# Performance work log

Measured on AMD Instinct MI355X. Metric: run time of the kernel, lower is better.

The kernel has to match this reference:

```python
import jax, jax.numpy as jnp
import numpy as np

B, S, D = 16, 1024, 1024   # batch, seq_len, dim_oculta
R, E = 512, 768            # n_riesgo lexicon entries, embedding dim
LN_EPS = 1e-5


def setup_inputs() -> dict:
    key = jax.random.key(0)
    ks = jax.random.split(key, 12)
    sd = 1.0 / np.sqrt(D)
    se = 1.0 / np.sqrt(E)
    return {
        "lstm_output": jax.random.normal(ks[0], (B, S, D), dtype=jnp.float32),
        "emb_riesgo": jax.random.normal(ks[1], (R, E), dtype=jnp.float32),
        "Wq": jax.random.normal(ks[2], (D, D), dtype=jnp.float32) * sd,
        "bq": jnp.zeros((D,), dtype=jnp.float32),
        "Wk": jax.random.normal(ks[3], (D, D), dtype=jnp.float32) * sd,
        "bk": jnp.zeros((D,), dtype=jnp.float32),
        "Wv": jax.random.normal(ks[4], (D, D), dtype=jnp.float32) * sd,
        "bv": jnp.zeros((D,), dtype=jnp.float32),
        "Wpr": jax.random.normal(ks[5], (E, D), dtype=jnp.float32) * se,
        "bpr": jnp.zeros((D,), dtype=jnp.float32),
        "escala": jnp.float32(1.0 / np.sqrt(D)),
        "gamma": jnp.ones((D,), dtype=jnp.float32),
        "beta": jnp.zeros((D,), dtype=jnp.float32),
    }


def reference(lstm_output, emb_riesgo, Wq, bq, Wk, bk, Wv, bv, Wpr, bpr,
              escala, gamma, beta):
    # Projections: [B,S,D]
    q = lstm_output @ Wq + bq
    k = lstm_output @ Wk + bk
    v = lstm_output @ Wv + bv

    # Risk lexicon projection: [R,D]
    riesgo_proy = emb_riesgo @ Wpr + bpr
    # Lexicon scores [B,S,R] -> max over lexicon -> sigmoid relevance [B,S,1]
    punt_lex = jnp.einsum('bsd,rd->bsr', q, riesgo_proy)
    relevancia = jax.nn.sigmoid(jnp.max(punt_lex, axis=-1, keepdims=True))

    # Hand-rolled self-attention
    scores = jnp.einsum('bsd,btd->bst', q, k) * escala   # [B,S,S]
    pesos = jax.nn.softmax(scores, axis=-1)
    contexto = jnp.einsum('bst,btd->bsd', pesos, v)      # [B,S,D]

    # Lexicon boost + LayerNorm over last dim
    x = contexto * (1.0 + relevancia)
    mu = jnp.mean(x, axis=-1, keepdims=True)
    var = jnp.mean(jnp.square(x - mu), axis=-1, keepdims=True)
    x = (x - mu) * jax.lax.rsqrt(var + LN_EPS) * gamma + beta

    # Mean pool over sequence -> [B,D]
    return jnp.mean(x, axis=1)
```

## Files before the change

### kernel.cpp

```cpp
#include <hip/hip_runtime.h>


#define BB 16
#define SS 1024
#define DD 1024
#define RR 512
#define EE 768

typedef __attribute__((ext_vector_type(4))) float f32x4;
typedef __attribute__((ext_vector_type(8))) __bf16 bf16x8;
typedef __attribute__((ext_vector_type(4))) unsigned int u32x4;

typedef __attribute__((address_space(1))) const void g_void;
typedef __attribute__((address_space(3))) void l_void;

__device__ __forceinline__ ushort f2b(float x) {
    unsigned u = __float_as_uint(x);
    u += 0x7fffu + ((u >> 16) & 1u);
    return (ushort)(u >> 16);
}

__global__ void cast_f32_bf16(const float* __restrict__ in, ushort* __restrict__ out, long n4) {
    long i = (long)blockIdx.x * blockDim.x + threadIdx.x;
    if (i >= n4) return;
    float4 v = *(const float4*)(in + i * 4);
    ushort4 o;
    o.x = f2b(v.x); o.y = f2b(v.y); o.z = f2b(v.z); o.w = f2b(v.w);
    *(ushort4*)(out + i * 4) = o;
}

__global__ void transpose_cast(const float* __restrict__ in, ushort* __restrict__ out,
                               int rows, int cols) {
    __shared__ float tile[32][33];
    const int bx = blockIdx.x * 32;
    const int by = blockIdx.y * 32;
    const int tx = threadIdx.x;
    const int ty = threadIdx.y;
#pragma unroll
    for (int i = 0; i < 32; i += 8)
        tile[ty + i][tx] = in[(long)(by + ty + i) * cols + bx + tx];
    __syncthreads();
#pragma unroll
    for (int i = 0; i < 32; i += 8)
        out[(long)(bx + ty + i) * rows + by + tx] = f2b(tile[tx][ty + i]);
}


#define VMWAIT(N) asm volatile("s_waitcnt vmcnt(" #N ")" ::: "memory")
#define BARRIER() asm volatile("s_barrier" ::: "memory")
#define LGKM0()   asm volatile("s_waitcnt lgkmcnt(0)" ::: "memory")
#define DSR(dst, addr, imm) \
    asm volatile("ds_read_b128 %0, %1 offset:" #imm : "=v"(dst) : "v"(addr))

#define STAGE(buf, mat, h, ti_) do {                                               \
    const int ti__ = (ti_) < (T - 1) ? (ti_) : (T - 1);                            \
    const ushort* sp__ = (mat) ? Bb : Ab;                                          \
    const long kb__ = (long)ti__ * 64 + scol;                                      \
    _Pragma("unroll")                                                              \
    for (int i__ = 0; i__ < 2; ++i__) {                                            \
        const int row0__ = (mat)                                                   \
            ? ((i__ * 2 + (wave >> 2)) * 64 + (h) * 32 + (wave & 3) * 8)           \
            : (i__ * 128 + (h) * 64 + wave * 8);                                   \
        __builtin_amdgcn_global_load_lds(                                          \
            (g_void*)(sp__ + (long)(row0__ + srow) * K + kb__),                    \
            (l_void*)(&lds[(buf) * 2 + (mat)][row0__ * 64]), 16, 0, 0);            \
    }                                                                              \
} while (0)

#define PHASE(curoff_, mh, nh, STAGE_STMT, WAIT_STMT) do {                         \
    if ((nh) == 0) {                                                               \
        const unsigned a0__ = abase0 + (curoff_) + (mh) * 8192;                    \
        const unsigned a1__ = abase1 + (curoff_) + (mh) * 8192;                    \
        DSR(af[0][0], a0__, 0);    DSR(af[0][1], a1__, 0);                         \
        DSR(af[1][0], a0__, 2048); DSR(af[1][1], a1__, 2048);                      \
        DSR(af[2][0], a0__, 4096); DSR(af[2][1], a1__, 4096);                      \
        DSR(af[3][0], a0__, 6144); DSR(af[3][1], a1__, 6144);                      \
    }                                                                              \
    {                                                                              \
        const unsigned b0__ = bbase0 + (curoff_) + (nh) * 4096;                    \
        const unsigned b1__ = bbase1 + (curoff_) + (nh) * 4096;                    \
        DSR(bfr[0][0], b0__, 0);    DSR(bfr[0][1], b1__, 0);                       \
        DSR(bfr[1][0], b0__, 2048); DSR(bfr[1][1], b1__, 2048);                    \
    }                                                                              \
    STAGE_STMT;                                                                    \
    BARRIER();                                                                     \
    LGKM0();                                                                       \
    __builtin_amdgcn_sched_barrier(0);                                             \
    __builtin_amdgcn_s_setprio(1);                                                 \
    _Pragma("unroll")                                                              \
    for (int mi = 0; mi < 4; ++mi)                                                 \
        _Pragma("unroll")                                                          \
        for (int ni = 0; ni < 2; ++ni) {                                           \
            acc[(mh) * 4 + mi][(nh) * 2 + ni] = __builtin_amdgcn_mfma_f32_16x16x32_bf16( \
                __builtin_bit_cast(bf16x8, af[mi][0]),                             \
                __builtin_bit_cast(bf16x8, bfr[ni][0]),                            \
                acc[(mh) * 4 + mi][(nh) * 2 + ni], 0, 0, 0);                       \
            acc[(mh) * 4 + mi][(nh) * 2 + ni] = __builtin_amdgcn_mfma_f32_16x16x32_bf16( \
                __builtin_bit_cast(bf16x8, af[mi][1]),                             \
                __builtin_bit_cast(bf16x8, bfr[ni][1]),                            \
                acc[(mh) * 4 + mi][(nh) * 2 + ni], 0, 0, 0);                       \
        }                                                                          \
    __builtin_amdgcn_s_setprio(0);                                                 \
    WAIT_STMT;                                                                     \
    BARRIER();                                                                     \
} while (0)

template <int BIAS_MODE, bool OUT_BF16, bool ROWSCALE>
__global__ __launch_bounds__(512, 2) void gemm8(
    const ushort* __restrict__ A, const ushort* __restrict__ B, void* __restrict__ C,
    const float* __restrict__ bias, const float* __restrict__ rowscale,
    const float* __restrict__ scale_ptr,
    int N, int K, int M, long sA, long sB, long sC)
{
    __shared__ ushort lds[4][16384];
    const int tid  = threadIdx.x;
    const int wave = tid >> 6;
    const int lane = tid & 63;
    const int wm = wave >> 2, wn = wave & 3;

    const int nx = gridDim.x, ny = gridDim.y;
    long flat = blockIdx.x + (long)nx * (blockIdx.y + (long)ny * blockIdx.z);
    const long nwg = (long)nx * ny * gridDim.z;
    const long cpx = nwg >> 3;
    flat = (flat & 7) * cpx + (flat >> 3);
    const int bn = (int)(flat % nx);
    const long r1 = flat / nx;
    const int bm = (int)(r1 % ny);
    const int bz = (int)(r1 / ny);

    const ushort* Ab = A + (long)bz * sA + (long)bm * 256 * K;
    const ushort* Bb = B + (long)bz * sB + (long)bn * 256 * K;
    const int T = K >> 6;

    const int srow = lane >> 3;
    const int scol = ((lane & 7) ^ srow) * 8;

    const unsigned lb = (unsigned)(unsigned long long)(void*)&lds[0][0];
    const int r15 = lane & 15;
    const int k0  = (lane >> 4) * 8;
    const int xo  = (lane & 7) * 8;
    const unsigned colA = (unsigned)((k0 ^ xo) * 2);
    const unsigned arow = (unsigned)((wm * 128 + r15) * 128);
    const unsigned brow = (unsigned)((wn * 64 + r15) * 128);
    const unsigned abase0 = lb + arow + colA;
    const unsigned abase1 = lb + arow + (colA ^ 64u);
    const unsigned bbase0 = lb + 32768u + brow + colA;
    const unsigned bbase1 = lb + 32768u + brow + (colA ^ 64u);

    f32x4 acc[8][4];
#pragma unroll
    for (int i = 0; i < 8; ++i)
#pragma unroll
        for (int j = 0; j < 4; ++j) acc[i][j] = (f32x4){0.f, 0.f, 0.f, 0.f};

    u32x4 af[4][2], bfr[2][2];

    STAGE(0, 0, 0, 0); STAGE(0, 1, 0, 0); STAGE(0, 0, 1, 0); STAGE(0, 1, 1, 0);
    STAGE(1, 0, 0, 1); STAGE(1, 1, 0, 1);
    VMWAIT(8);
    BARRIER();

    for (int t = 0; t < T; ++t) {
        const int cur = t & 1, nxt = cur ^ 1;
        const unsigned curoff = cur ? 65536u : 0u;
        PHASE(curoff, 0, 0, STAGE(nxt, 0, 1, t + 1), VMWAIT(6));
        PHASE(curoff, 0, 1, STAGE(nxt, 1, 1, t + 1), (void)0);
        PHASE(curoff, 1, 0, STAGE(cur, 0, 0, t + 2), (void)0);
        PHASE(curoff, 1, 1, STAGE(cur, 1, 0, t + 2), VMWAIT(8));
    }
    VMWAIT(0);

    const float scale = scale_ptr ? *scale_ptr : 1.0f;
    const int g4 = (lane >> 4) * 4;
#pragma unroll
    for (int mi = 0; mi < 8; ++mi) {
        const int row0 = bm * 256 + wm * 128 + mi * 16 + g4;
#pragma unroll
        for (int ni = 0; ni < 4; ++ni) {
            const int col = bn * 256 + wn * 64 + ni * 16 + r15;
            float bcol = (BIAS_MODE == 1) ? bias[col] : 0.0f;
#pragma unroll
            for (int j = 0; j < 4; ++j) {
                float v = acc[mi][ni][j] * scale;
                if (BIAS_MODE == 1) v += bcol;
                if (BIAS_MODE == 2) v += bias[row0 + j];
                if (ROWSCALE)       v *= rowscale[(long)bz * M + row0 + j];
                const long idx = (long)bz * sC + (long)(row0 + j) * N + col;
                if (OUT_BF16) ((ushort*)C)[idx] = f2b(v);
                else          ((float*)C)[idx]  = v;
            }
        }
    }
}

__global__ void rowmax_boost(const float* __restrict__ punt, float* __restrict__ boost) {
    const long row = blockIdx.x;
    const int tid = threadIdx.x;
    __shared__ float sm[4];
    float m = fmaxf(punt[row * RR + tid], punt[row * RR + tid + 256]);
#pragma unroll
    for (int o = 32; o > 0; o >>= 1) m = fmaxf(m, __shfl_down(m, o));
    if ((tid & 63) == 0) sm[tid >> 6] = m;
    __syncthreads();
    if (tid == 0) {
        m = fmaxf(fmaxf(sm[0], sm[1]), fmaxf(sm[2], sm[3]));
        boost[row] = 1.0f + 1.0f / (1.0f + __expf(-m));
    }
}

__global__ void softmax_rows(const float* __restrict__ S, ushort* __restrict__ P) {
    const long row = blockIdx.x;
    const int tid = threadIdx.x;
    __shared__ float sm[4];
    float4 x = *(const float4*)(S + row * 1024 + tid * 4);
    float m = fmaxf(fmaxf(x.x, x.y), fmaxf(x.z, x.w));
#pragma unroll
    for (int o = 32; o > 0; o >>= 1) m = fmaxf(m, __shfl_down(m, o));
    if ((tid & 63) == 0) sm[tid >> 6] = m;
    __syncthreads();
    m = fmaxf(fmaxf(sm[0], sm[1]), fmaxf(sm[2], sm[3]));
    __syncthreads();
    float e0 = __expf(x.x - m), e1 = __expf(x.y - m);
    float e2 = __expf(x.z - m), e3 = __expf(x.w - m);
    float s = e0 + e1 + e2 + e3;
#pragma unroll
    for (int o = 32; o > 0; o >>= 1) s += __shfl_down(s, o);
    if ((tid & 63) == 0) sm[tid >> 6] = s;
    __syncthreads();
    s = sm[0] + sm[1] + sm[2] + sm[3];
    const float inv = 1.0f / s;
    ushort4 o4;
    o4.x = f2b(e0 * inv); o4.y = f2b(e1 * inv);
    o4.z = f2b(e2 * inv); o4.w = f2b(e3 * inv);
    *(ushort4*)(P + row * 1024 + tid * 4) = o4;
}

__global__ void ln_pool(const float* __restrict__ x, const float* __restrict__ gamma,
                        const float* __restrict__ beta, float* __restrict__ out) {
    const int b = blockIdx.y, chunk = blockIdx.x, tid = threadIdx.x;
    __shared__ float sm[8];
    float4 g  = *(const float4*)(gamma + tid * 4);
    float4 be = *(const float4*)(beta + tid * 4);
    float a0 = 0, a1 = 0, a2 = 0, a3 = 0;
    for (int s = chunk * 64; s < chunk * 64 + 64; ++s) {
        float4 xv = *(const float4*)(x + ((long)b * SS + s) * DD + tid * 4);
        float ls = xv.x + xv.y + xv.z + xv.w;
        float lq = xv.x * xv.x + xv.y * xv.y + xv.z * xv.z + xv.w * xv.w;
#pragma unroll
        for (int o = 32; o > 0; o >>= 1) { ls += __shfl_down(ls, o); lq += __shfl_down(lq, o); }
        if ((tid & 63) == 0) { sm[(tid >> 6) * 2] = ls; sm[(tid >> 6) * 2 + 1] = lq; }
        __syncthreads();
        const float ts = sm[0] + sm[2] + sm[4] + sm[6];
        const float tq = sm[1] + sm[3] + sm[5] + sm[7];
        __syncthreads();
        const float mu  = ts * (1.0f / DD);
        const float var = tq * (1.0f / DD) - mu * mu;
        const float rs  = rsqrtf(var + 1e-5f);
        a0 += (xv.x - mu) * rs * g.x + be.x;
        a1 += (xv.y - mu) * rs * g.y + be.y;
        a2 += (xv.z - mu) * rs * g.z + be.z;
        a3 += (xv.w - mu) * rs * g.w + be.w;
    }
    const float is = 1.0f / SS;
    atomicAdd(out + (long)b * DD + tid * 4 + 0, a0 * is);
    atomicAdd(out + (long)b * DD + tid * 4 + 1, a1 * is);
    atomicAdd(out + (long)b * DD + tid * 4 + 2, a2 * is);
    atomicAdd(out + (long)b * DD + tid * 4 + 3, a3 * is);
}

#define OFF_XBF   0ul
#define OFF_WQT   33554432ul
#define OFF_WKT   35651584ul
#define OFF_WVT   37748736ul
#define OFF_WPRT  39845888ul
#define OFF_EMBB  41418752ul
#define OFF_Q     42205184ul
#define OFF_K     75759616ul
#define OFF_VT    109314048ul
#define OFF_RP    142868480ul
#define OFF_BOOST 143917056ul
#define OFF_BIG   143982592ul

extern "C" void kernel_launch(void* const* d_in, const int* in_sizes, int n_in,
                              void* d_out, int out_size, void* d_ws, size_t ws_size,
                              hipStream_t stream) {
    (void)in_sizes; (void)n_in; (void)ws_size;
    const float* lstm  = (const float*)d_in[0];
    const float* emb   = (const float*)d_in[1];
    const float* Wq    = (const float*)d_in[2];
    const float* bq    = (const float*)d_in[3];
    const float* Wk    = (const float*)d_in[4];
    const float* bk    = (const float*)d_in[5];
    const float* Wv    = (const float*)d_in[6];
    const float* bv    = (const float*)d_in[7];
    const float* Wpr   = (const float*)d_in[8];
    const float* bpr   = (const float*)d_in[9];
    const float* esc   = (const float*)d_in[10];
    const float* gamma = (const float*)d_in[11];
    const float* beta  = (const float*)d_in[12];
    float* out = (float*)d_out;

    char* ws = (char*)d_ws;
    ushort* Xbf  = (ushort*)(ws + OFF_XBF);
    ushort* Wqt  = (ushort*)(ws + OFF_WQT);
    ushort* Wkt  = (ushort*)(ws + OFF_WKT);
    ushort* Wvt  = (ushort*)(ws + OFF_WVT);
    ushort* Wprt = (ushort*)(ws + OFF_WPRT);
    ushort* Embb = (ushort*)(ws + OFF_EMBB);
    ushort* Qb   = (ushort*)(ws + OFF_Q);
    ushort* Kb   = (ushort*)(ws + OFF_K);
    ushort* Vt   = (ushort*)(ws + OFF_VT);
    ushort* Rp   = (ushort*)(ws + OFF_RP);
    float*  boost= (float*)(ws + OFF_BOOST);
    float*  big  = (float*)(ws + OFF_BIG);
    ushort* P    = (ushort*)(ws + OFF_XBF);

    hipMemsetAsync(d_out, 0, (size_t)out_size * sizeof(float), stream);

    {
        long n4 = (long)BB * SS * DD / 4;
        cast_f32_bf16<<<dim3((n4 + 255) / 256), dim3(256), 0, stream>>>(lstm, Xbf, n4);
        long e4 = (long)RR * EE / 4;
        cast_f32_bf16<<<dim3((e4 + 255) / 256), dim3(256), 0, stream>>>(emb, Embb, e4);
        transpose_cast<<<dim3(32, 32), dim3(32, 8), 0, stream>>>(Wq, Wqt, 1024, 1024);
        transpose_cast<<<dim3(32, 32), dim3(32, 8), 0, stream>>>(Wk, Wkt, 1024, 1024);
        transpose_cast<<<dim3(32, 32), dim3(32, 8), 0, stream>>>(Wv, Wvt, 1024, 1024);
        transpose_cast<<<dim3(32, 24), dim3(32, 8), 0, stream>>>(Wpr, Wprt, 768, 1024);
    }

    gemm8<1, true, false><<<dim3(4, 2, 1), 512, 0, stream>>>(
        Embb, Wprt, Rp, bpr, nullptr, nullptr, 1024, 768, 512, 0, 0, 0);
    gemm8<1, true, false><<<dim3(4, 64, 1), 512, 0, stream>>>(
        Xbf, Wqt, Qb, bq, nullptr, nullptr, 1024, 1024, 16384, 0, 0, 0);
    gemm8<1, true, false><<<dim3(4, 64, 1), 512, 0, stream>>>(
        Xbf, Wkt, Kb, bk, nullptr, nullptr, 1024, 1024, 16384, 0, 0, 0);
    gemm8<2, true, false><<<dim3(4, 4, 16), 512, 0, stream>>>(
        Wvt, Xbf, Vt, bv, nullptr, nullptr, 1024, 1024, 1024,
        0, (long)SS * DD, (long)DD * SS);
    gemm8<0, false, false><<<dim3(2, 64, 1), 512, 0, stream>>>(
        Qb, Rp, big, nullptr, nullptr, nullptr, 512, 1024, 16384, 0, 0, 0);
    rowmax_boost<<<dim3(16384), 256, 0, stream>>>(big, boost);
    gemm8<0, false, false><<<dim3(4, 4, 16), 512, 0, stream>>>(
        Qb, Kb, big, nullptr, nullptr, esc, 1024, 1024, 1024,
        (long)SS * DD, (long)SS * DD, (long)SS * SS);
    softmax_rows<<<dim3(16384), 256, 0, stream>>>(big, P);
    gemm8<0, false, true><<<dim3(4, 4, 16), 512, 0, stream>>>(
        P, Vt, big, nullptr, boost, nullptr, 1024, 1024, 1024,
        (long)SS * SS, (long)DD * SS, (long)SS * DD);
    ln_pool<<<dim3(16, 16), 256, 0, stream>>>(big, gamma, beta, out);
}
```

Before: 458.9 us.

## Store intermediate score/context matrices as bf16 and reorder GEMM phase fragment reuse

The lexicon scores, attention scores and boosted context are now written as bf16 instead of fp32. Rowmax, softmax and LayerNorm-pool read them as bf16, which halves the traffic on these large [B,S,S] and [B,S,D] intermediates. Separately, the GEMM inner loop keeps both B-fragment halves in registers and reorders its phases (0,0 / 0,1 / 1,1 / 1,0), so A and B LDS reads are reused across phases and one LDS wait is skipped. This costs precision: scores are rounded to bf16 before softmax, and the context is rounded before LayerNorm. It also raises register pressure in the GEMM.

Result: faster. 439.2 us (-4.3%).

```diff
diff --git a/kernel.cpp b/kernel.cpp
--- a/kernel.cpp
+++ b/kernel.cpp
@@ -18,6 +18,9 @@
     unsigned u = __float_as_uint(x);
     u += 0x7fffu + ((u >> 16) & 1u);
     return (ushort)(u >> 16);
+}
+__device__ __forceinline__ float b2f(ushort u) {
+    return __uint_as_float((unsigned)u << 16);
 }
 
 __global__ void cast_f32_bf16(const float* __restrict__ in, ushort* __restrict__ out, long n4) {
@@ -67,8 +70,8 @@
     }                                                                              \
 } while (0)
 
-#define PHASE(curoff_, mh, nh, STAGE_STMT, WAIT_STMT) do {                         \
-    if ((nh) == 0) {                                                               \
+#define PHASE(curoff_, mh, nh, RA, RB, STAGE_STMT, WAIT_STMT, LG) do {             \
+    if (RA) {                                                                      \
         const unsigned a0__ = abase0 + (curoff_) + (mh) * 8192;                    \
         const unsigned a1__ = abase1 + (curoff_) + (mh) * 8192;                    \
         DSR(af[0][0], a0__, 0);    DSR(af[0][1], a1__, 0);                         \
@@ -76,16 +79,15 @@
         DSR(af[2][0], a0__, 4096); DSR(af[2][1], a1__, 4096);                      \
         DSR(af[3][0], a0__, 6144); DSR(af[3][1], a1__, 6144);                      \
     }                                                                              \
-    {                                                                              \
+    if (RB) {                                                                      \
         const unsigned b0__ = bbase0 + (curoff_) + (nh) * 4096;                    \
         const unsigned b1__ = bbase1 + (curoff_) + (nh) * 4096;                    \
-        DSR(bfr[0][0], b0__, 0);    DSR(bfr[0][1], b1__, 0);                       \
-        DSR(bfr[1][0], b0__, 2048); DSR(bfr[1][1], b1__, 2048);                    \
+        DSR(bfr[nh][0][0], b0__, 0);    DSR(bfr[nh][0][1], b1__, 0);               \
+        DSR(bfr[nh][1][0], b0__, 2048); DSR(bfr[nh][1][1], b1__, 2048);            \
     }                                                                              \
     STAGE_STMT;                                                                    \
     BARRIER();                                                                     \
-    LGKM0();                                                                       \
-    __builtin_amdgcn_sched_barrier(0);                                             \
+    if (LG) { LGKM0(); __builtin_amdgcn_sched_barrier(0); }                        \
     __builtin_amdgcn_s_setprio(1);                                                 \
     _Pragma("unroll")                                                              \
     for (int mi = 0; mi < 4; ++mi)                                                 \
@@ -93,11 +95,11 @@
         for (int ni = 0; ni < 2; ++ni) {                                           \
             acc[(mh) * 4 + mi][(nh) * 2 + ni] = __builtin_amdgcn_mfma_f32_16x16x32_bf16( \
                 __builtin_bit_cast(bf16x8, af[mi][0]),                             \
-                __builtin_bit_cast(bf16x8, bfr[ni][0]),                            \
+                __builtin_bit_cast(bf16x8, bfr[nh][ni][0]),                        \
                 acc[(mh) * 4 + mi][(nh) * 2 + ni], 0, 0, 0);                       \
             acc[(mh) * 4 + mi][(nh) * 2 + ni] = __builtin_amdgcn_mfma_f32_16x16x32_bf16( \
                 __builtin_bit_cast(bf16x8, af[mi][1]),                             \
-                __builtin_bit_cast(bf16x8, bfr[ni][1]),                            \
+                __builtin_bit_cast(bf16x8, bfr[nh][ni][1]),                        \
                 acc[(mh) * 4 + mi][(nh) * 2 + ni], 0, 0, 0);                       \
         }                                                                          \
     __builtin_amdgcn_s_setprio(0);                                                 \
@@ -153,9 +155,9 @@
 #pragma unroll
         for (int j = 0; j < 4; ++j) acc[i][j] = (f32x4){0.f, 0.f, 0.f, 0.f};
 
-    u32x4 af[4][2], bfr[2][2];
-
-    STAGE(0, 0, 0, 0); STAGE(0, 1, 0, 0); STAGE(0, 0, 1, 0); STAGE(0, 1, 1, 0);
+    u32x4 af[4][2], bfr[2][2][2];
+
+    STAGE(0, 0, 0, 0); STAGE(0, 1, 0, 0); STAGE(0, 1, 1, 0); STAGE(0, 0, 1, 0);
     STAGE(1, 0, 0, 1); STAGE(1, 1, 0, 1);
     VMWAIT(8);
     BARRIER();
@@ -163,10 +165,10 @@
     for (int t = 0; t < T; ++t) {
         const int cur = t & 1, nxt = cur ^ 1;
         const unsigned curoff = cur ? 65536u : 0u;
-        PHASE(curoff, 0, 0, STAGE(nxt, 0, 1, t + 1), VMWAIT(6));
-        PHASE(curoff, 0, 1, STAGE(nxt, 1, 1, t + 1), (void)0);
-        PHASE(curoff, 1, 0, STAGE(cur, 0, 0, t + 2), (void)0);
-        PHASE(curoff, 1, 1, STAGE(cur, 1, 0, t + 2), VMWAIT(8));
+        PHASE(curoff, 0, 0, 1, 1, STAGE(nxt, 0, 1, t + 1), VMWAIT(6), 1);
+        PHASE(curoff, 0, 1, 0, 1, STAGE(nxt, 1, 1, t + 1), (void)0, 1);
+        PHASE(curoff, 1, 1, 1, 0, STAGE(cur, 0, 0, t + 2), (void)0, 1);
+        PHASE(curoff, 1, 0, 0, 0, STAGE(cur, 1, 0, t + 2), VMWAIT(8), 0);
     }
     VMWAIT(0);
 
@@ -193,11 +195,12 @@
     }
 }
 
-__global__ void rowmax_boost(const float* __restrict__ punt, float* __restrict__ boost) {
+__global__ void rowmax_boost(const ushort* __restrict__ punt, float* __restrict__ boost) {
     const long row = blockIdx.x;
     const int tid = threadIdx.x;
     __shared__ float sm[4];
-    float m = fmaxf(punt[row * RR + tid], punt[row * RR + tid + 256]);
+    ushort2 p2 = *(const ushort2*)(punt + row * RR + tid * 2);
+    float m = fmaxf(b2f(p2.x), b2f(p2.y));
 #pragma unroll
     for (int o = 32; o > 0; o >>= 1) m = fmaxf(m, __shfl_down(m, o));
     if ((tid & 63) == 0) sm[tid >> 6] = m;
@@ -208,20 +211,21 @@
     }
 }
 
-__global__ void softmax_rows(const float* __restrict__ S, ushort* __restrict__ P) {
+__global__ void softmax_rows(const ushort* __restrict__ S, ushort* __restrict__ P) {
     const long row = blockIdx.x;
     const int tid = threadIdx.x;
     __shared__ float sm[4];
-    float4 x = *(const float4*)(S + row * 1024 + tid * 4);
-    float m = fmaxf(fmaxf(x.x, x.y), fmaxf(x.z, x.w));
+    ushort4 xr = *(const ushort4*)(S + row * 1024 + tid * 4);
+    float x0 = b2f(xr.x), x1 = b2f(xr.y), x2 = b2f(xr.z), x3 = b2f(xr.w);
+    float m = fmaxf(fmaxf(x0, x1), fmaxf(x2, x3));
 #pragma unroll
     for (int o = 32; o > 0; o >>= 1) m = fmaxf(m, __shfl_down(m, o));
     if ((tid & 63) == 0) sm[tid >> 6] = m;
     __syncthreads();
     m = fmaxf(fmaxf(sm[0], sm[1]), fmaxf(sm[2], sm[3]));
     __syncthreads();
-    float e0 = __expf(x.x - m), e1 = __expf(x.y - m);
-    float e2 = __expf(x.z - m), e3 = __expf(x.w - m);
+    float e0 = __expf(x0 - m), e1 = __expf(x1 - m);
+    float e2 = __expf(x2 - m), e3 = __expf(x3 - m);
     float s = e0 + e1 + e2 + e3;
 #pragma unroll
     for (int o = 32; o > 0; o >>= 1) s += __shfl_down(s, o);
@@ -235,7 +239,7 @@
     *(ushort4*)(P + row * 1024 + tid * 4) = o4;
 }
 
-__global__ void ln_pool(const float* __restrict__ x, const float* __restrict__ gamma,
+__global__ void ln_pool(const ushort* __restrict__ x, const float* __restrict__ gamma,
                         const float* __restrict__ beta, float* __restrict__ out) {
     const int b = blockIdx.y, chunk = blockIdx.x, tid = threadIdx.x;
     __shared__ float sm[8];
@@ -243,9 +247,10 @@
     float4 be = *(const float4*)(beta + tid * 4);
     float a0 = 0, a1 = 0, a2 = 0, a3 = 0;
     for (int s = chunk * 64; s < chunk * 64 + 64; ++s) {
-        float4 xv = *(const float4*)(x + ((long)b * SS + s) * DD + tid * 4);
-        float ls = xv.x + xv.y + xv.z + xv.w;
-        float lq = xv.x * xv.x + xv.y * xv.y + xv.z * xv.z + xv.w * xv.w;
+        ushort4 xr = *(const ushort4*)(x + ((long)b * SS + s) * DD + tid * 4);
+        float x0 = b2f(xr.x), x1 = b2f(xr.y), x2 = b2f(xr.z), x3 = b2f(xr.w);
+        float ls = x0 + x1 + x2 + x3;
+        float lq = x0 * x0 + x1 * x1 + x2 * x2 + x3 * x3;
 #pragma unroll
         for (int o = 32; o > 0; o >>= 1) { ls += __shfl_down(ls, o); lq += __shfl_down(lq, o); }
         if ((tid & 63) == 0) { sm[(tid >> 6) * 2] = ls; sm[(tid >> 6) * 2 + 1] = lq; }
@@ -256,10 +261,10 @@
         const float mu  = ts * (1.0f / DD);
         const float var = tq * (1.0f / DD) - mu * mu;
         const float rs  = rsqrtf(var + 1e-5f);
-        a0 += (xv.x - mu) * rs * g.x + be.x;
-        a1 += (xv.y - mu) * rs * g.y + be.y;
-        a2 += (xv.z - mu) * rs * g.z + be.z;
-        a3 += (xv.w - mu) * rs * g.w + be.w;
+        a0 += (x0 - mu) * rs * g.x + be.x;
+        a1 += (x1 - mu) * rs * g.y + be.y;
+        a2 += (x2 - mu) * rs * g.z + be.z;
+        a3 += (x3 - mu) * rs * g.w + be.w;
     }
     const float is = 1.0f / SS;
     atomicAdd(out + (long)b * DD + tid * 4 + 0, a0 * is);
@@ -312,7 +317,7 @@
     ushort* Vt   = (ushort*)(ws + OFF_VT);
     ushort* Rp   = (ushort*)(ws + OFF_RP);
     float*  boost= (float*)(ws + OFF_BOOST);
-    float*  big  = (float*)(ws + OFF_BIG);
+    ushort* bigU = (ushort*)(ws + OFF_BIG);
     ushort* P    = (ushort*)(ws + OFF_XBF);
 
     hipMemsetAsync(d_out, 0, (size_t)out_size * sizeof(float), stream);
@@ -337,15 +342,15 @@
     gemm8<2, true, false><<<dim3(4, 4, 16), 512, 0, stream>>>(
         Wvt, Xbf, Vt, bv, nullptr, nullptr, 1024, 1024, 1024,
         0, (long)SS * DD, (long)DD * SS);
-    gemm8<0, false, false><<<dim3(2, 64, 1), 512, 0, stream>>>(
-        Qb, Rp, big, nullptr, nullptr, nullptr, 512, 1024, 16384, 0, 0, 0);
-    rowmax_boost<<<dim3(16384), 256, 0, stream>>>(big, boost);
-    gemm8<0, false, false><<<dim3(4, 4, 16), 512, 0, stream>>>(
-        Qb, Kb, big, nullptr, nullptr, esc, 1024, 1024, 1024,
+    gemm8<0, true, false><<<dim3(2, 64, 1), 512, 0, stream>>>(
+        Qb, Rp, bigU, nullptr, nullptr, nullptr, 512, 1024, 16384, 0, 0, 0);
+    rowmax_boost<<<dim3(16384), 256, 0, stream>>>(bigU, boost);
+    gemm8<0, true, false><<<dim3(4, 4, 16), 512, 0, stream>>>(
+        Qb, Kb, bigU, nullptr, nullptr, esc, 1024, 1024, 1024,
         (long)SS * DD, (long)SS * DD, (long)SS * SS);
-    softmax_rows<<<dim3(16384), 256, 0, stream>>>(big, P);
-    gemm8<0, false, true><<<dim3(4, 4, 16), 512, 0, stream>>>(
-        P, Vt, big, nullptr, boost, nullptr, 1024, 1024, 1024,
+    softmax_rows<<<dim3(16384), 256, 0, stream>>>(bigU, P);
+    gemm8<0, true, true><<<dim3(4, 4, 16), 512, 0, stream>>>(
+        P, Vt, bigU, nullptr, boost, nullptr, 1024, 1024, 1024,
         (long)SS * SS, (long)DD * SS, (long)SS * DD);
-    ln_pool<<<dim3(16, 16), 256, 0, stream>>>(big, gamma, beta, out);
-}
+    ln_pool<<<dim3(16, 16), 256, 0, stream>>>(bigU, gamma, beta, out);
+}
```
